# Kernel optimization log

Measured on AMD Instinct MI355X. Metric: run time of the kernel, lower is better.

## Reference

```python
import jax, jax.numpy as jnp
import numpy as np

NUM_LAYERS = 2
NUM_RES_LAYERS = 1  # residual add applied to layers i >= NUM_LAYERS - NUM_RES_LAYERS


def _lstm_seq(x, W, U, b, reverse):
    """Keras-style LSTM over full sequence. x:[B,T,E], W:[E,4H], U:[H,4H], b:[4H].
    Gate order i,f,g,o (Keras). reverse=True emulates go_backwards + K.reverse
    (lax.scan reverse=True keeps outputs time-aligned). Returns [B,T,H]."""
    B = x.shape[0]
    H = U.shape[0]
    # precompute input projections for all timesteps in one big matmul
    zx = jnp.einsum('bte,eg->btg', x, W) + b  # [B,T,4H]
    zx = jnp.swapaxes(zx, 0, 1)  # [T,B,4H]

    def step(carry, zxt):
        h, c = carry
        z = zxt + h @ U  # [B,4H]
        i, f, g, o = jnp.split(z, 4, axis=-1)
        i = jax.nn.sigmoid(i)
        f = jax.nn.sigmoid(f)
        g = jnp.tanh(g)
        o = jax.nn.sigmoid(o)
        c = f * c + i * g
        h = o * jnp.tanh(c)
        return (h, c), h

    init = (jnp.zeros((B, H), x.dtype), jnp.zeros((B, H), x.dtype))
    _, hs = jax.lax.scan(step, init, zx, reverse=reverse)  # [T,B,H]
    return jnp.swapaxes(hs, 0, 1)


def setup_inputs() -> dict:
    key = jax.random.key(0)
    k1, k2, k3 = jax.random.split(key, 3)
    B, T, E, H = 512, 200, 128, 128
    s = 0.05  # keep gates in a sane regime
    x = jax.random.normal(k1, (B, T, E), dtype=jnp.float32)
    W = jax.random.normal(k2, (NUM_LAYERS, 2, E, 4 * H), dtype=jnp.float32) * s
    U = jax.random.normal(k3, (NUM_LAYERS, 2, H, 4 * H), dtype=jnp.float32) * s
    b = jnp.ones((NUM_LAYERS, 2, 4 * H), dtype=jnp.float32)  # bias_initializer='ones'
    return {"x": x, "W": W, "U": U, "b": b}


def reference(x, W, U, b):
    # inference mode: dropout inactive
    input_fw = x
    input_bw = x
    for i in range(NUM_LAYERS):
        out_fw = _lstm_seq(input_fw, W[i, 0], U[i, 0], b[i, 0], reverse=False)
        out_bw = _lstm_seq(input_bw, W[i, 1], U[i, 1], b[i, 1], reverse=True)
        if i >= NUM_LAYERS - NUM_RES_LAYERS:
            out_fw = out_fw + input_fw
            out_bw = out_bw + input_bw
        input_fw = out_fw
        input_bw = out_bw
    # mode == 'ave'
    return (input_fw + input_bw) / 2
```

## Files before the change

### kernel.cpp

```cpp
#include <hip/hip_runtime.h>
#include <math.h>


typedef _Float16 f16;
typedef _Float16 f16x4 __attribute__((ext_vector_type(4)));
typedef _Float16 f16x8 __attribute__((ext_vector_type(8)));
typedef float    f32x4 __attribute__((ext_vector_type(4)));

#define B_   512
#define T_   200
#define E_   128
#define H_   128
#define G4_  512
#define M_   (B_*T_)
#define LUTN 8192

static __device__ __forceinline__ void lgkm_barrier() {
  asm volatile("s_waitcnt lgkmcnt(0)" ::: "memory");
  __builtin_amdgcn_s_barrier();
}

__global__ __launch_bounds__(256)
void cvt_x(const float* __restrict__ x, f16* __restrict__ xh) {
  const int n8 = M_ * E_ / 8;
  for (int i = blockIdx.x * 256 + threadIdx.x; i < n8; i += gridDim.x * 256) {
    const float4 a = ((const float4*)x)[i * 2];
    const float4 b = ((const float4*)x)[i * 2 + 1];
    f16x8 v;
    v[0] = (f16)a.x; v[1] = (f16)a.y; v[2] = (f16)a.z; v[3] = (f16)a.w;
    v[4] = (f16)b.x; v[5] = (f16)b.y; v[6] = (f16)b.z; v[7] = (f16)b.w;
    *(f16x8*)(xh + (size_t)i * 8) = v;
  }
}

__global__ __launch_bounds__(256)
void prep_w(const float* __restrict__ W, const float* __restrict__ U,
            f16* __restrict__ Wt, f16* __restrict__ Ut) {
  const int m = blockIdx.x;
  const float* s = (m < 4 ? W + (size_t)m * E_ * G4_ : U + (size_t)(m - 4) * E_ * G4_);
  f16* d        = (m < 4 ? Wt + (size_t)m * E_ * G4_ : Ut + (size_t)(m - 4) * E_ * G4_);
  for (int i = threadIdx.x; i < E_ * G4_; i += 256) {
    const int k = i >> 9, g = i & 511;
    float v = s[i];
    if ((g >> 7) == 2) v *= 2.f;
    d[(size_t)g * E_ + k] = (f16)v;
  }
}

template <int LAYER>
__global__ __launch_bounds__(512, 2)
void scan_fused(const f16* __restrict__ in,
                const f16* __restrict__ Utl,
                const f16* __restrict__ Wtl,
                const float* __restrict__ bl,
                const f16* __restrict__ res,
                f16* __restrict__ hout)
{
  __shared__ float lut[LUTN];
  __shared__ f16 hsh[2][16][136];

  const int tid  = threadIdx.x;
  const int lane = tid & 63;
  const int wv   = tid >> 6;
  const int row  = lane & 15;
  const int kg   = lane >> 4;
  const int bx   = blockIdx.x;
  const int dir  = bx >> 5;
  const int R0   = (bx & 31) * 16;
  const int coff = wv * 16 + kg * 4;

  const f16* Ud = Utl + (size_t)dir * G4_ * E_;
  const f16* Wd = Wtl + (size_t)dir * G4_ * E_;
  const float* bd = bl + (size_t)dir * G4_;
  const f16* ind  = in + (LAYER == 1 ? (size_t)dir * M_ * H_ : 0);
  f16* houtd      = hout + (size_t)dir * M_ * H_;

  for (int i = tid; i < LUTN; i += 512) {
    const float xx = (float)(i - LUTN / 2) * (1.f / 256.f);
    lut[i] = 1.f / (1.f + expf(-xx));
  }
  for (int i = tid; i < 2 * 16 * 136; i += 512) ((f16*)hsh)[i] = (f16)0.f;

  f16x8 aU[4][4], aW[4][4];
#pragma unroll
  for (int g = 0; g < 4; ++g) {
    const size_t gcol = (size_t)(g * 128 + wv * 16 + row) * E_;
#pragma unroll
    for (int kk = 0; kk < 4; ++kk) {
      aU[g][kk] = *(const f16x8*)(Ud + gcol + kk * 32 + kg * 8);
      aW[g][kk] = *(const f16x8*)(Wd + gcol + kk * 32 + kg * 8);
    }
  }
  f32x4 zb[4];
#pragma unroll
  for (int g = 0; g < 4; ++g) {
#pragma unroll
    for (int i = 0; i < 4; ++i) {
      const float v = bd[g * 128 + coff + i];
      zb[g][i] = (g == 2) ? 2.f * v : v;
    }
  }

  const int t0 = dir ? (T_ - 1) : 0;
  const int ts = dir ? -1 : 1;

  const f16* inrow  = ind + (size_t)(R0 + row) * T_ * E_;
  const f16* resrow = (LAYER == 1)
      ? res + (size_t)dir * M_ * H_ + (size_t)(R0 + row) * T_ * H_ : nullptr;
  f16* outrow = houtd + (size_t)(R0 + row) * T_ * H_;

  float cc[4] = {0.f, 0.f, 0.f, 0.f};

  f16x8 xP[4], xA[4], xB[4];
  f16x4 rvA = {}, rvB = {};
#pragma unroll
  for (int kk = 0; kk < 4; ++kk) {
    xP[kk] = *(const f16x8*)(inrow + (long)t0 * E_ + kk * 32 + kg * 8);
    xA[kk] = *(const f16x8*)(inrow + (long)(t0 + ts) * E_ + kk * 32 + kg * 8);
    xB[kk] = *(const f16x8*)(inrow + (long)(t0 + 2 * ts) * E_ + kk * 32 + kg * 8);
  }
  if (LAYER == 1) {
    rvA = *(const f16x4*)(resrow + (long)t0 * H_ + coff);
    rvB = *(const f16x4*)(resrow + (long)(t0 + ts) * H_ + coff);
  }

  lgkm_barrier();

  f32x4 zA[4], zB[4];
#pragma unroll
  for (int g = 0; g < 4; ++g) zA[g] = zb[g];
#pragma unroll
  for (int kk = 0; kk < 4; ++kk) {
    zA[0] = __builtin_amdgcn_mfma_f32_16x16x32_f16(aW[0][kk], xP[kk], zA[0], 0, 0, 0);
    zA[1] = __builtin_amdgcn_mfma_f32_16x16x32_f16(aW[1][kk], xP[kk], zA[1], 0, 0, 0);
    zA[2] = __builtin_amdgcn_mfma_f32_16x16x32_f16(aW[2][kk], xP[kk], zA[2], 0, 0, 0);
    zA[3] = __builtin_amdgcn_mfma_f32_16x16x32_f16(aW[3][kk], xP[kk], zA[3], 0, 0, 0);
  }

  auto step = [&](f32x4 (&zc)[4], f32x4 (&zn)[4], f16x8 (&xn)[4], f16x4& rv,
                  int s, int rp, int wp) {
    const int t = t0 + s * ts;

    f16x8 hf[4];
#pragma unroll
    for (int kk = 0; kk < 4; ++kk) hf[kk] = *(const f16x8*)&hsh[rp][row][kk * 32 + kg * 8];

#pragma unroll
    for (int kk = 0; kk < 4; ++kk) {
      zc[0] = __builtin_amdgcn_mfma_f32_16x16x32_f16(aU[0][kk], hf[kk], zc[0], 0, 0, 0);
      zc[1] = __builtin_amdgcn_mfma_f32_16x16x32_f16(aU[1][kk], hf[kk], zc[1], 0, 0, 0);
      zc[2] = __builtin_amdgcn_mfma_f32_16x16x32_f16(aU[2][kk], hf[kk], zc[2], 0, 0, 0);
      zc[3] = __builtin_amdgcn_mfma_f32_16x16x32_f16(aU[3][kk], hf[kk], zc[3], 0, 0, 0);
    }

#pragma unroll
    for (int g = 0; g < 4; ++g) zn[g] = zb[g];
#pragma unroll
    for (int kk = 0; kk < 4; ++kk) {
      zn[0] = __builtin_amdgcn_mfma_f32_16x16x32_f16(aW[0][kk], xn[kk], zn[0], 0, 0, 0);
      zn[1] = __builtin_amdgcn_mfma_f32_16x16x32_f16(aW[1][kk], xn[kk], zn[1], 0, 0, 0);
      zn[2] = __builtin_amdgcn_mfma_f32_16x16x32_f16(aW[2][kk], xn[kk], zn[2], 0, 0, 0);
      zn[3] = __builtin_amdgcn_mfma_f32_16x16x32_f16(aW[3][kk], xn[kk], zn[3], 0, 0, 0);
    }

    {
      const f16* p = inrow + (long)(t + 3 * ts) * E_;
#pragma unroll
      for (int kk = 0; kk < 4; ++kk) xn[kk] = *(const f16x8*)(p + kk * 32 + kg * 8);
    }
    float rvf[4];
    if (LAYER == 1) {
#pragma unroll
      for (int i = 0; i < 4; ++i) rvf[i] = (float)rv[i];
      rv = *(const f16x4*)(resrow + (long)(t + 2 * ts) * H_ + coff);
    }

    auto lidx = [](float u) -> int {
      u = fminf(fmaxf(u, 0.f), (float)(LUTN - 1));
      return (int)u;
    };
    float hv[4];
#pragma unroll
    for (int i = 0; i < 4; ++i) {
      const float ig = lut[lidx(fmaf(zc[0][i], 256.f, (float)(LUTN / 2)))];
      const float fg = lut[lidx(fmaf(zc[1][i], 256.f, (float)(LUTN / 2)))];
      const float gg = fmaf(2.f, lut[lidx(fmaf(zc[2][i], 256.f, (float)(LUTN / 2)))], -1.f);
      const float og = lut[lidx(fmaf(zc[3][i], 256.f, (float)(LUTN / 2)))];
      cc[i] = fg * cc[i] + ig * gg;
      const float th = fmaf(2.f, lut[lidx(fmaf(cc[i], 512.f, (float)(LUTN / 2)))], -1.f);
      hv[i] = og * th;
    }

    f16x4 hp;
#pragma unroll
    for (int i = 0; i < 4; ++i) hp[i] = (f16)hv[i];
    *(f16x4*)&hsh[wp][row][coff] = hp;

    f16* orow = outrow + (long)t * H_ + coff;
    if (LAYER == 0) {
      *(f16x4*)orow = hp;
    } else {
      f16x4 o;
#pragma unroll
      for (int i = 0; i < 4; ++i) o[i] = (f16)(0.5f * (hv[i] + rvf[i]));
      *(f16x4*)orow = o;
    }

    lgkm_barrier();
  };

  for (int k = 0; k < T_ / 2; ++k) {
    step(zA, zB, xA, rvA, 2 * k,     0, 1);
    step(zB, zA, xB, rvB, 2 * k + 1, 1, 0);
  }
}

__global__ __launch_bounds__(256)
void final_add(const f16* __restrict__ a, const f16* __restrict__ b,
               float* __restrict__ o)
{
  const int n8 = M_ * H_ / 8;
  for (int i = blockIdx.x * 256 + threadIdx.x; i < n8; i += gridDim.x * 256) {
    const f16x8 va = *(const f16x8*)(a + (size_t)i * 8);
    const f16x8 vb = *(const f16x8*)(b + (size_t)i * 8);
    float4 o0, o1;
    o0.x = (float)va[0] + (float)vb[0];  o0.y = (float)va[1] + (float)vb[1];
    o0.z = (float)va[2] + (float)vb[2];  o0.w = (float)va[3] + (float)vb[3];
    o1.x = (float)va[4] + (float)vb[4];  o1.y = (float)va[5] + (float)vb[5];
    o1.z = (float)va[6] + (float)vb[6];  o1.w = (float)va[7] + (float)vb[7];
    *(float4*)(o + (size_t)i * 8)     = o0;
    *(float4*)(o + (size_t)i * 8 + 4) = o1;
  }
}

extern "C" void kernel_launch(void* const* d_in, const int* in_sizes, int n_in,
                              void* d_out, int out_size, void* d_ws, size_t ws_size,
                              hipStream_t stream) {
  const float* x = (const float*)d_in[0];
  const float* W = (const float*)d_in[1];
  const float* U = (const float*)d_in[2];
  const float* b = (const float*)d_in[3];
  float* out = (float*)d_out;

  char* ws = (char*)d_ws;
  f16* xh = (f16*)(ws + 2048);
  f16* h0 = xh + (size_t)M_ * E_;
  f16* h1 = h0 + (size_t)2 * M_ * H_;
  f16* Wt = h1 + (size_t)2 * M_ * H_;
  f16* Ut = Wt + (size_t)4 * G4_ * E_;

  const size_t WTL = (size_t)2 * G4_ * E_;
  const size_t BL  = 2 * G4_;

  cvt_x<<<dim3(2048), 256, 0, stream>>>(x, xh);
  prep_w<<<dim3(8), 256, 0, stream>>>(W, U, Wt, Ut);
  scan_fused<0><<<dim3(64), 512, 0, stream>>>(xh, Ut, Wt, b, nullptr, h0);
  scan_fused<1><<<dim3(64), 512, 0, stream>>>(h0, Ut + WTL, Wt + WTL, b + BL, h0, h1);
  final_add<<<dim3(2048), 256, 0, stream>>>(h1, h1 + (size_t)M_ * H_, out);
}
```

Baseline: 618.5 us.

## Replace LDS sigmoid LUT with exp2/rcp intrinsics and reorder MFMA issue

Removes the 32KB shared-memory sigmoid lookup table and computes the gates with hardware exp2 and reciprocal instructions. This cuts LDS gather traffic on the serial recurrence and shrinks shared memory use. The input-projection MFMAs for the next step are now issued before the recurrent MFMAs. The step uses incrementing pointers, packed f16 conversion and half-precision residual averaging, and the workspace buffers get small padding offsets. The trade is more transcendental ALU work per gate, a slight change in precision, and the residual average now rounded in f16.

```diff
diff --git a/kernel.cpp b/kernel.cpp
--- a/kernel.cpp
+++ b/kernel.cpp
@@ -1,8 +1,8 @@
 #include <hip/hip_runtime.h>
-#include <math.h>
 
 
 typedef _Float16 f16;
+typedef _Float16 f16x2 __attribute__((ext_vector_type(2)));
 typedef _Float16 f16x4 __attribute__((ext_vector_type(4)));
 typedef _Float16 f16x8 __attribute__((ext_vector_type(8)));
 typedef float    f32x4 __attribute__((ext_vector_type(4)));
@@ -13,7 +13,24 @@
 #define H_   128
 #define G4_  512
 #define M_   (B_*T_)
-#define LUTN 8192
+
+static __device__ __forceinline__ float rcpa(float x) {
+#if __has_builtin(__builtin_amdgcn_rcpf)
+  return __builtin_amdgcn_rcpf(x);
+#else
+  return 1.f / x;
+#endif
+}
+static __device__ __forceinline__ float exp2a(float x) {
+#if __has_builtin(__builtin_amdgcn_exp2f)
+  return __builtin_amdgcn_exp2f(x);
+#else
+  return exp2f(x);
+#endif
+}
+static __device__ __forceinline__ f16x2 pk2(float lo, float hi) {
+  return __builtin_bit_cast(f16x2, __builtin_amdgcn_cvt_pkrtz(lo, hi));
+}
 
 static __device__ __forceinline__ void lgkm_barrier() {
   asm volatile("s_waitcnt lgkmcnt(0)" ::: "memory");
@@ -56,7 +73,6 @@
                 const f16* __restrict__ res,
                 f16* __restrict__ hout)
 {
-  __shared__ float lut[LUTN];
   __shared__ f16 hsh[2][16][136];
 
   const int tid  = threadIdx.x;
@@ -75,12 +91,6 @@
   const f16* ind  = in + (LAYER == 1 ? (size_t)dir * M_ * H_ : 0);
   f16* houtd      = hout + (size_t)dir * M_ * H_;
 
-  for (int i = tid; i < LUTN; i += 512) {
-    const float xx = (float)(i - LUTN / 2) * (1.f / 256.f);
-    lut[i] = 1.f / (1.f + expf(-xx));
-  }
-  for (int i = tid; i < 2 * 16 * 136; i += 512) ((f16*)hsh)[i] = (f16)0.f;
-
   f16x8 aU[4][4], aW[4][4];
 #pragma unroll
   for (int g = 0; g < 4; ++g) {
@@ -101,49 +111,78 @@
     }
   }
 
+  for (int i = tid; i < 2 * 16 * 136; i += 512) ((f16*)hsh)[i] = (f16)0.f;
+
   const int t0 = dir ? (T_ - 1) : 0;
   const int ts = dir ? -1 : 1;
 
-  const f16* inrow  = ind + (size_t)(R0 + row) * T_ * E_;
+  const f16* inrow  = ind + (size_t)(R0 + row) * T_ * E_ + kg * 8;
   const f16* resrow = (LAYER == 1)
-      ? res + (size_t)dir * M_ * H_ + (size_t)(R0 + row) * T_ * H_ : nullptr;
-  f16* outrow = houtd + (size_t)(R0 + row) * T_ * H_;
-
-  float cc[4] = {0.f, 0.f, 0.f, 0.f};
-
-  f16x8 xP[4], xA[4], xB[4];
-  f16x4 rvA = {}, rvB = {};
+      ? res + (size_t)dir * M_ * H_ + (size_t)(R0 + row) * T_ * H_ + coff : nullptr;
+  f16* outptr = houtd + (size_t)(R0 + row) * T_ * H_ + (size_t)t0 * H_ + coff;
+
+  float cc0 = 0.f, cc1 = 0.f, cc2 = 0.f, cc3 = 0.f;
+
+  const f16* xptrA = inrow + (long)(t0 + ts) * E_;
+  const f16* xptrB = inrow + (long)(t0 + 2 * ts) * E_;
+  f16x8 xpA[4], xpB[4], xP[4];
 #pragma unroll
   for (int kk = 0; kk < 4; ++kk) {
-    xP[kk] = *(const f16x8*)(inrow + (long)t0 * E_ + kk * 32 + kg * 8);
-    xA[kk] = *(const f16x8*)(inrow + (long)(t0 + ts) * E_ + kk * 32 + kg * 8);
-    xB[kk] = *(const f16x8*)(inrow + (long)(t0 + 2 * ts) * E_ + kk * 32 + kg * 8);
-  }
+    xP[kk]  = *(const f16x8*)(inrow + (long)t0 * E_ + kk * 32);
+    xpA[kk] = *(const f16x8*)(xptrA + kk * 32);
+    xpB[kk] = *(const f16x8*)(xptrB + kk * 32);
+  }
+  const f16* rptrA = nullptr; const f16* rptrB = nullptr;
+  uint2 rvA = {}, rvB = {};
   if (LAYER == 1) {
-    rvA = *(const f16x4*)(resrow + (long)t0 * H_ + coff);
-    rvB = *(const f16x4*)(resrow + (long)(t0 + ts) * H_ + coff);
+    rptrA = resrow + (long)t0 * H_;
+    rptrB = resrow + (long)(t0 + ts) * H_;
+    rvA = *(const uint2*)rptrA;
+    rvB = *(const uint2*)rptrB;
   }
 
   lgkm_barrier();
 
   f32x4 zA[4], zB[4];
 #pragma unroll
-  for (int g = 0; g < 4; ++g) zA[g] = zb[g];
-#pragma unroll
-  for (int kk = 0; kk < 4; ++kk) {
-    zA[0] = __builtin_amdgcn_mfma_f32_16x16x32_f16(aW[0][kk], xP[kk], zA[0], 0, 0, 0);
-    zA[1] = __builtin_amdgcn_mfma_f32_16x16x32_f16(aW[1][kk], xP[kk], zA[1], 0, 0, 0);
-    zA[2] = __builtin_amdgcn_mfma_f32_16x16x32_f16(aW[2][kk], xP[kk], zA[2], 0, 0, 0);
-    zA[3] = __builtin_amdgcn_mfma_f32_16x16x32_f16(aW[3][kk], xP[kk], zA[3], 0, 0, 0);
-  }
-
-  auto step = [&](f32x4 (&zc)[4], f32x4 (&zn)[4], f16x8 (&xn)[4], f16x4& rv,
-                  int s, int rp, int wp) {
-    const int t = t0 + s * ts;
-
+  for (int g = 0; g < 4; ++g) {
+    zA[g] = __builtin_amdgcn_mfma_f32_16x16x32_f16(aW[g][0], xP[0], zb[g], 0, 0, 0);
+#pragma unroll
+    for (int kk = 1; kk < 4; ++kk)
+      zA[g] = __builtin_amdgcn_mfma_f32_16x16x32_f16(aW[g][kk], xP[kk], zA[g], 0, 0, 0);
+  }
+
+  constexpr float NL2E  = -1.4426950408889634f;
+  constexpr float NL2E2 = -2.8853900817779268f;
+
+  auto step = [&](f32x4 (&zc)[4], f32x4 (&zn)[4], f16x8 (&xp)[4],
+                  const f16*& xptr, uint2& rv, const f16*& rptr,
+                  int rp, int wp) {
     f16x8 hf[4];
 #pragma unroll
     for (int kk = 0; kk < 4; ++kk) hf[kk] = *(const f16x8*)&hsh[rp][row][kk * 32 + kg * 8];
+
+#pragma unroll
+    for (int g = 0; g < 4; ++g)
+      zn[g] = __builtin_amdgcn_mfma_f32_16x16x32_f16(aW[g][0], xp[0], zb[g], 0, 0, 0);
+#pragma unroll
+    for (int kk = 1; kk < 4; ++kk) {
+      zn[0] = __builtin_amdgcn_mfma_f32_16x16x32_f16(aW[0][kk], xp[kk], zn[0], 0, 0, 0);
+      zn[1] = __builtin_amdgcn_mfma_f32_16x16x32_f16(aW[1][kk], xp[kk], zn[1], 0, 0, 0);
+      zn[2] = __builtin_amdgcn_mfma_f32_16x16x32_f16(aW[2][kk], xp[kk], zn[2], 0, 0, 0);
+      zn[3] = __builtin_amdgcn_mfma_f32_16x16x32_f16(aW[3][kk], xp[kk], zn[3], 0, 0, 0);
+    }
+
+    xptr += 2 * ts * E_;
+#pragma unroll
+    for (int kk = 0; kk < 4; ++kk) xp[kk] = *(const f16x8*)(xptr + kk * 32);
+    f16x2 rva, rvb;
+    if (LAYER == 1) {
+      rva = __builtin_bit_cast(f16x2, rv.x);
+      rvb = __builtin_bit_cast(f16x2, rv.y);
+      rptr += 2 * ts * H_;
+      rv = *(const uint2*)rptr;
+    }
 
 #pragma unroll
     for (int kk = 0; kk < 4; ++kk) {
@@ -153,65 +192,51 @@
       zc[3] = __builtin_amdgcn_mfma_f32_16x16x32_f16(aU[3][kk], hf[kk], zc[3], 0, 0, 0);
     }
 
-#pragma unroll
-    for (int g = 0; g < 4; ++g) zn[g] = zb[g];
-#pragma unroll
-    for (int kk = 0; kk < 4; ++kk) {
-      zn[0] = __builtin_amdgcn_mfma_f32_16x16x32_f16(aW[0][kk], xn[kk], zn[0], 0, 0, 0);
-      zn[1] = __builtin_amdgcn_mfma_f32_16x16x32_f16(aW[1][kk], xn[kk], zn[1], 0, 0, 0);
-      zn[2] = __builtin_amdgcn_mfma_f32_16x16x32_f16(aW[2][kk], xn[kk], zn[2], 0, 0, 0);
-      zn[3] = __builtin_amdgcn_mfma_f32_16x16x32_f16(aW[3][kk], xn[kk], zn[3], 0, 0, 0);
-    }
-
-    {
-      const f16* p = inrow + (long)(t + 3 * ts) * E_;
-#pragma unroll
-      for (int kk = 0; kk < 4; ++kk) xn[kk] = *(const f16x8*)(p + kk * 32 + kg * 8);
-    }
-    float rvf[4];
-    if (LAYER == 1) {
-#pragma unroll
-      for (int i = 0; i < 4; ++i) rvf[i] = (float)rv[i];
-      rv = *(const f16x4*)(resrow + (long)(t + 2 * ts) * H_ + coff);
-    }
-
-    auto lidx = [](float u) -> int {
-      u = fminf(fmaxf(u, 0.f), (float)(LUTN - 1));
-      return (int)u;
-    };
     float hv[4];
+    float cc[4] = {cc0, cc1, cc2, cc3};
 #pragma unroll
     for (int i = 0; i < 4; ++i) {
-      const float ig = lut[lidx(fmaf(zc[0][i], 256.f, (float)(LUTN / 2)))];
-      const float fg = lut[lidx(fmaf(zc[1][i], 256.f, (float)(LUTN / 2)))];
-      const float gg = fmaf(2.f, lut[lidx(fmaf(zc[2][i], 256.f, (float)(LUTN / 2)))], -1.f);
-      const float og = lut[lidx(fmaf(zc[3][i], 256.f, (float)(LUTN / 2)))];
-      cc[i] = fg * cc[i] + ig * gg;
-      const float th = fmaf(2.f, lut[lidx(fmaf(cc[i], 512.f, (float)(LUTN / 2)))], -1.f);
-      hv[i] = og * th;
-    }
-
-    f16x4 hp;
-#pragma unroll
-    for (int i = 0; i < 4; ++i) hp[i] = (f16)hv[i];
-    *(f16x4*)&hsh[wp][row][coff] = hp;
-
-    f16* orow = outrow + (long)t * H_ + coff;
+      const float ei = exp2a(zc[0][i] * NL2E);
+      const float ef = exp2a(zc[1][i] * NL2E);
+      const float eg = exp2a(zc[2][i] * NL2E);
+      const float eo = exp2a(zc[3][i] * NL2E);
+      const float ig = rcpa(1.f + ei);
+      const float fg = rcpa(1.f + ef);
+      const float gg = fmaf(2.f, rcpa(1.f + eg), -1.f);
+      const float og = rcpa(1.f + eo);
+      cc[i] = fmaf(fg, cc[i], ig * gg);
+      const float ec = exp2a(cc[i] * NL2E2);
+      const float tc = fmaf(2.f, rcpa(1.f + ec), -1.f);
+      hv[i] = og * tc;
+    }
+    cc0 = cc[0]; cc1 = cc[1]; cc2 = cc[2]; cc3 = cc[3];
+
+    const f16x2 h01 = pk2(hv[0], hv[1]);
+    const f16x2 h23 = pk2(hv[2], hv[3]);
+    uint2 hp;
+    hp.x = __builtin_bit_cast(unsigned int, h01);
+    hp.y = __builtin_bit_cast(unsigned int, h23);
+    *(uint2*)&hsh[wp][row][coff] = hp;
+
     if (LAYER == 0) {
-      *(f16x4*)orow = hp;
+      *(uint2*)outptr = hp;
     } else {
-      f16x4 o;
-#pragma unroll
-      for (int i = 0; i < 4; ++i) o[i] = (f16)(0.5f * (hv[i] + rvf[i]));
-      *(f16x4*)orow = o;
-    }
+      const f16x2 half2 = {(f16)0.5f, (f16)0.5f};
+      const f16x2 o01 = (h01 + rva) * half2;
+      const f16x2 o23 = (h23 + rvb) * half2;
+      uint2 o;
+      o.x = __builtin_bit_cast(unsigned int, o01);
+      o.y = __builtin_bit_cast(unsigned int, o23);
+      *(uint2*)outptr = o;
+    }
+    outptr += ts * H_;
 
     lgkm_barrier();
   };
 
   for (int k = 0; k < T_ / 2; ++k) {
-    step(zA, zB, xA, rvA, 2 * k,     0, 1);
-    step(zB, zA, xB, rvB, 2 * k + 1, 1, 0);
+    step(zA, zB, xpA, xptrA, rvA, rptrA, 0, 1);
+    step(zB, zA, xpB, xptrB, rvB, rptrB, 1, 0);
   }
 }
 
@@ -244,9 +269,9 @@
 
   char* ws = (char*)d_ws;
   f16* xh = (f16*)(ws + 2048);
-  f16* h0 = xh + (size_t)M_ * E_;
-  f16* h1 = h0 + (size_t)2 * M_ * H_;
-  f16* Wt = h1 + (size_t)2 * M_ * H_;
+  f16* h0 = xh + (size_t)M_ * E_ + 1024;
+  f16* h1 = h0 + (size_t)2 * M_ * H_ + 1024;
+  f16* Wt = h1 + (size_t)2 * M_ * H_ + 1024;
   f16* Ut = Wt + (size_t)4 * G4_ * E_;
 
   const size_t WTL = (size_t)2 * G4_ * E_;
```

Result: slower. 636.1 us (+2.9%).
